# Performance work log

Hardware: AMD Instinct MI355X
Metric: run time of the kernel (lower is better)

Reference implementation:

```python
import math
import jax, jax.numpy as jnp
import numpy as np

D_MODEL = 1024
N_HEADS = 16
D_K = D_MODEL // N_HEADS


def _alibi_slopes(n_heads):
    # Faithful to the torch _get_slopes: slopes[i] = 2**(-8 + i), subsampled if
    # n_heads is not a power of two.
    power = 2 ** math.ceil(math.log2(n_heads))
    slopes = np.array([2.0 ** (-8 + i) for i in range(power)], dtype=np.float32)
    if n_heads != power:
        ratio = power // n_heads
        slopes = slopes[np.arange(0, power, ratio)][:n_heads]
    return jnp.asarray(slopes)


def setup_inputs() -> dict:
    key = jax.random.key(0)
    ks = jax.random.split(key, 11)
    B, S, D = 2, 2048, D_MODEL
    w = 0.02  # weight init scale
    return {
        "query": jax.random.normal(ks[0], (B, S, D), jnp.float32),
        "key": jax.random.normal(ks[1], (B, S, D), jnp.float32),
        "value": jax.random.normal(ks[2], (B, S, D), jnp.float32),
        "Wq": jax.random.normal(ks[3], (D, D), jnp.float32) * w,
        "bq": jax.random.normal(ks[4], (D,), jnp.float32) * w,
        "Wk": jax.random.normal(ks[5], (D, D), jnp.float32) * w,
        "bk": jax.random.normal(ks[6], (D,), jnp.float32) * w,
        "Wv": jax.random.normal(ks[7], (D, D), jnp.float32) * w,
        "bv": jax.random.normal(ks[8], (D,), jnp.float32) * w,
        "Wo": jax.random.normal(ks[9], (D, D), jnp.float32) * w,
        "bo": jax.random.normal(ks[10], (D,), jnp.float32) * w,
    }


def reference(query, key, value, Wq, bq, Wk, bk, Wv, bv, Wo, bo):
    B, Sq, D = query.shape
    Sk = key.shape[1]
    H, dk = N_HEADS, D_K

    # projections (torch Linear: x @ W.T + b)
    q = (query @ Wq.T + bq).reshape(B, Sq, H, dk).transpose(0, 2, 1, 3)  # [B,H,Sq,dk]
    k = (key @ Wk.T + bk).reshape(B, Sk, H, dk).transpose(0, 2, 1, 3)    # [B,H,Sk,dk]
    v = (value @ Wv.T + bv).reshape(B, Sk, H, dk).transpose(0, 2, 1, 3)  # [B,H,Sk,dk]

    scores = jnp.einsum("bhqd,bhkd->bhqk", q, k) / jnp.sqrt(jnp.float32(dk))

    # ALiBi bias: slopes[h] * (i - j), non-causal path (is_causal=False)
    dist = (jnp.arange(Sq)[:, None] - jnp.arange(Sk)[None, :]).astype(scores.dtype)
    slopes = _alibi_slopes(H)
    scores = scores + slopes[None, :, None, None] * dist[None, None, :, :]

    attn = jax.nn.softmax(scores, axis=-1)
    out = jnp.einsum("bhqk,bhkd->bhqd", attn, v)          # [B,H,Sq,dk]
    out = out.transpose(0, 2, 1, 3).reshape(B, Sq, D)     # [B,Sq,D]
    return out @ Wo.T + bo
```

## Files before the change

### kernel.cpp

```cpp
#include <hip/hip_runtime.h>

typedef __bf16 bf16_t;
typedef bf16_t bf16x8 __attribute__((ext_vector_type(8)));
typedef float f32x4 __attribute__((ext_vector_type(4)));
typedef float f32x16 __attribute__((ext_vector_type(16)));
typedef unsigned short u16x4 __attribute__((ext_vector_type(4)));
typedef unsigned int u32x4v __attribute__((ext_vector_type(4)));
typedef unsigned int u32;

#define DEV static __device__ __forceinline__


DEV unsigned short f2bf(float f) {
  unsigned int u = __builtin_bit_cast(unsigned int, f);
  u = (u + 0x7fffu + ((u >> 16) & 1u)) >> 16;
  return (unsigned short)u;
}

DEV float fexp2(float x) {
  float r;
  asm("v_exp_f32 %0, %1" : "=v"(r) : "v"(x));
  return r;
}

DEV u32 cvtpk(float lo, float hi_) {
  u32 r;
  asm("v_cvt_pk_bf16_f32 %0, %1, %2" : "=v"(r) : "v"(lo), "v"(hi_));
  return r;
}

DEV void plswap(u32& a, u32& b) {
  asm("v_permlane32_swap_b32 %0, %1" : "+v"(a), "+v"(b));
}

DEV void async_ld16(const unsigned short* gsrc, unsigned short* lbase, int lane) {
#if __has_builtin(__builtin_amdgcn_global_load_lds)
  __builtin_amdgcn_global_load_lds(
      (const __attribute__((address_space(1))) unsigned int*)(const void*)gsrc,
      (__attribute__((address_space(3))) unsigned int*)(void*)lbase, 16, 0, 0);
#else
  *reinterpret_cast<u32x4v*>(reinterpret_cast<char*>(lbase) + lane * 16) =
      *reinterpret_cast<const u32x4v*>(gsrc);
#endif
}


DEV void cvt_body(const float* __restrict__ src, unsigned short* __restrict__ dst, int i) {
  const float4* s = reinterpret_cast<const float4*>(src) + (size_t)i * 2;
  float4 a = s[0], c = s[1];
  u16x4 lo = {f2bf(a.x), f2bf(a.y), f2bf(a.z), f2bf(a.w)};
  u16x4 hi = {f2bf(c.x), f2bf(c.y), f2bf(c.z), f2bf(c.w)};
  u16x4* d = reinterpret_cast<u16x4*>(dst) + (size_t)i * 2;
  d[0] = lo;
  d[1] = hi;
}

__global__ __launch_bounds__(256) void cvt_qkv(const float* __restrict__ q,
                                               const float* __restrict__ k,
                                               const float* __restrict__ v,
                                               unsigned short* dq, unsigned short* dk,
                                               unsigned short* dv) {
  const int i = blockIdx.x * 256 + threadIdx.x;
  const float* src = blockIdx.z == 0 ? q : blockIdx.z == 1 ? k : v;
  unsigned short* dst = blockIdx.z == 0 ? dq : blockIdx.z == 1 ? dk : dv;
  cvt_body(src, dst, i);
}

__global__ __launch_bounds__(256) void cvt_w(const float* __restrict__ a,
                                             const float* __restrict__ b,
                                             const float* __restrict__ c,
                                             const float* __restrict__ d, unsigned short* da,
                                             unsigned short* db_, unsigned short* dc,
                                             unsigned short* dd) {
  const int i = blockIdx.x * 256 + threadIdx.x;
  const float* src = blockIdx.z == 0 ? a : blockIdx.z == 1 ? b : blockIdx.z == 2 ? c : d;
  unsigned short* dst = blockIdx.z == 0 ? da : blockIdx.z == 1 ? db_ : blockIdx.z == 2 ? dc : dd;
  cvt_body(src, dst, i);
}


DEV void stage_tile_128x64(const unsigned short* __restrict__ G, int row0, int k0,
                           unsigned short* lbuf, int lane, int wv) {
#pragma unroll
  for (int r = 0; r < 4; ++r) {
    const int rowA = (r * 4 + wv) * 8 + (lane >> 3);
    const int chunk = (lane & 7) ^ (rowA & 7);
    const unsigned short* gsrc = G + (size_t)(row0 + rowA) * 1024 + k0 + chunk * 8;
    unsigned short* lbase = lbuf + (r * 4 + wv) * 512;
    async_ld16(gsrc, lbase, lane);
  }
}

DEV void gemm_core(const unsigned short* __restrict__ X, const unsigned short* __restrict__ W,
                   unsigned short* lA, unsigned short* lB, int bm0, int bn0, int lane, int wv,
                   int wm, int wn, f32x4 acc[4][4]) {
  for (int kt = 0; kt < 16; ++kt) {
    __syncthreads();
    stage_tile_128x64(X, bm0, kt * 64, lA, lane, wv);
    stage_tile_128x64(W, bn0, kt * 64, lB, lane, wv);
    __syncthreads();
#pragma unroll
    for (int kk = 0; kk < 2; ++kk) {
      bf16x8 af[4], bfr[4];
#pragma unroll
      for (int f = 0; f < 4; ++f) {
        const int rowA = wm * 64 + f * 16 + (lane & 15);
        const int cA = (kk * 4 + (lane >> 4)) ^ (rowA & 7);
        af[f] = *reinterpret_cast<const bf16x8*>(lA + rowA * 64 + cA * 8);
        const int rowB = wn * 64 + f * 16 + (lane & 15);
        const int cB = (kk * 4 + (lane >> 4)) ^ (rowB & 7);
        bfr[f] = *reinterpret_cast<const bf16x8*>(lB + rowB * 64 + cB * 8);
      }
#pragma unroll
      for (int i = 0; i < 4; ++i)
#pragma unroll
        for (int j = 0; j < 4; ++j)
          acc[i][j] = __builtin_amdgcn_mfma_f32_16x16x32_bf16(af[i], bfr[j], acc[i][j], 0, 0, 0);
    }
  }
}


__global__ __launch_bounds__(256) void gemm_qkv_kernel(
    const unsigned short* __restrict__ Xq, const unsigned short* __restrict__ Xk,
    const unsigned short* __restrict__ Xv, const unsigned short* __restrict__ Wq,
    const unsigned short* __restrict__ Wk, const unsigned short* __restrict__ Wv,
    const float* __restrict__ bq, const float* __restrict__ bk, const float* __restrict__ bv,
    unsigned short* __restrict__ Qp, unsigned short* __restrict__ Kp,
    unsigned short* __restrict__ Vp) {
  __shared__ unsigned short lA[128 * 64];
  __shared__ unsigned short lB[128 * 64];
  const unsigned short* X;
  const unsigned short* W;
  const float* bias;
  unsigned short* dst;
  if (blockIdx.z == 0) { X = Xq; W = Wq; bias = bq; dst = Qp; }
  else if (blockIdx.z == 1) { X = Xk; W = Wk; bias = bk; dst = Kp; }
  else { X = Xv; W = Wv; bias = bv; dst = Vp; }
  const bool zV = (blockIdx.z == 2);
  const int lane = threadIdx.x & 63, wv = threadIdx.x >> 6;
  const int wm = wv >> 1, wn = wv & 1;
  const int bm0 = blockIdx.x * 128, bn0 = blockIdx.y * 128;
  f32x4 acc[4][4] = {};
  gemm_core(X, W, lA, lB, bm0, bn0, lane, wv, wm, wn, acc);
#pragma unroll
  for (int i = 0; i < 4; ++i) {
    const int mbase = bm0 + wm * 64 + i * 16 + ((lane >> 4) << 2);
#pragma unroll
    for (int j = 0; j < 4; ++j) {
      const int n = bn0 + wn * 64 + j * 16 + (lane & 15);
      const float bia = bias[n];
      const int h = n >> 6, d = n & 63;
#pragma unroll
      for (int r = 0; r < 4; ++r) {
        const int m = mbase + r;
        const int b = m >> 11, s = m & 2047;
        const unsigned short val = f2bf(acc[i][j][r] + bia);
        if (zV)
          dst[((size_t)(b * 16 + h) * 64 + d) * 2048 + s] = val;
        else
          dst[((size_t)(b * 16 + h) * 2048 + s) * 64 + d] = val;
      }
    }
  }
}


__global__ __launch_bounds__(256) void gemm_out_kernel(const unsigned short* __restrict__ X,
                                                       const unsigned short* __restrict__ W,
                                                       const float* __restrict__ bias,
                                                       float* __restrict__ out) {
  __shared__ unsigned short lA[128 * 64];
  __shared__ unsigned short lB[128 * 64];
  const int lane = threadIdx.x & 63, wv = threadIdx.x >> 6;
  const int wm = wv >> 1, wn = wv & 1;
  const int bm0 = blockIdx.x * 128, bn0 = blockIdx.y * 128;
  f32x4 acc[4][4] = {};
  gemm_core(X, W, lA, lB, bm0, bn0, lane, wv, wm, wn, acc);
#pragma unroll
  for (int i = 0; i < 4; ++i) {
    const int mbase = bm0 + wm * 64 + i * 16 + ((lane >> 4) << 2);
#pragma unroll
    for (int j = 0; j < 4; ++j) {
      const int n = bn0 + wn * 64 + j * 16 + (lane & 15);
      const float bia = bias[n];
#pragma unroll
      for (int r = 0; r < 4; ++r) out[(size_t)(mbase + r) * 1024 + n] = acc[i][j][r] + bia;
    }
  }
}


__global__ __launch_bounds__(256) void knorm_kernel(const unsigned short* __restrict__ Kp,
                                                    unsigned* __restrict__ nb2) {
  const int bh = blockIdx.y;
  const int s = blockIdx.x * 256 + threadIdx.x;
  const u32x4v* row = reinterpret_cast<const u32x4v*>(Kp + ((size_t)bh * 2048 + s) * 64);
  float ss = 0.0f;
#pragma unroll
  for (int c = 0; c < 8; ++c) {
    u32x4v u = row[c];
#pragma unroll
    for (int e = 0; e < 4; ++e) {
      const float lo = __builtin_bit_cast(float, u[e] << 16);
      const float hi = __builtin_bit_cast(float, u[e] & 0xFFFF0000u);
      ss = __builtin_fmaf(lo, lo, ss);
      ss = __builtin_fmaf(hi, hi, ss);
    }
  }
#pragma unroll
  for (int off = 1; off <= 32; off <<= 1) ss = fmaxf(ss, __shfl_xor(ss, off));
  if ((threadIdx.x & 63) == 0) atomicMax(nb2 + bh, __float_as_uint(ss));
}


__global__ __launch_bounds__(128) void attn_prepass(const unsigned short* __restrict__ Qp,
                                                    const unsigned short* __restrict__ Kp,
                                                    const unsigned* __restrict__ nb2,
                                                    float* __restrict__ mfA,
                                                    float* __restrict__ bltA) {
  __shared__ float sred[4];
  const int lane = threadIdx.x & 63, wv = threadIdx.x >> 6;
  const int lq = lane & 31, hi = lane >> 5;
  const int qt = blockIdx.x, bh = blockIdx.y, h = bh & 15;
  const float L2E = 1.4426950408889634f;
  const float slope2 = ldexpf(L2E, h - 8);
  const float SC2 = 0.125f * L2E;
  const size_t headoff = (size_t)bh * 2048 * 64;
  const unsigned short* Qh = Qp + headoff;
  const unsigned short* Kh = Kp + headoff;
  const int q_glob = qt * 64 + wv * 32 + lq;

  bf16x8 qf[4];
#pragma unroll
  for (int tt = 0; tt < 4; ++tt)
    qf[tt] = *reinterpret_cast<const bf16x8*>(Qh + (size_t)q_glob * 64 + tt * 16 + hi * 8);

  float qq = 0.0f;
#pragma unroll
  for (int tt = 0; tt < 4; ++tt)
#pragma unroll
    for (int e = 0; e < 8; ++e) {
      const float x = (float)qf[tt][e];
      qq = __builtin_fmaf(x, x, qq);
    }
  qq += __shfl_xor(qq, 32);
#pragma unroll
  for (int off = 1; off <= 16; off <<= 1) qq = fmaxf(qq, __shfl_xor(qq, off));

  f32x16 s0 = {}, s1 = {};
#pragma unroll
  for (int tt = 0; tt < 4; ++tt) {
    bf16x8 k0 = *reinterpret_cast<const bf16x8*>(Kh + (size_t)lq * 64 + tt * 16 + hi * 8);
    s0 = __builtin_amdgcn_mfma_f32_32x32x16_bf16(k0, qf[tt], s0, 0, 0, 0);
    bf16x8 k1 = *reinterpret_cast<const bf16x8*>(Kh + (size_t)(32 + lq) * 64 + tt * 16 + hi * 8);
    s1 = __builtin_amdgcn_mfma_f32_32x32x16_bf16(k1, qf[tt], s1, 0, 0, 0);
  }
  float zmax = -3.0e38f;
#pragma unroll
  for (int r = 0; r < 16; ++r) {
    const float cb = -slope2 * (float)(4 * hi + (r & 3) + 8 * (r >> 2));
    const float x0 = __builtin_fmaf(s0[r], SC2, cb);
    const float x1 = __builtin_fmaf(s1[r], SC2, cb - slope2 * 32.0f);
    zmax = fmaxf(zmax, fmaxf(x0, x1));
  }
  zmax = fmaxf(zmax, __shfl_xor(zmax, 32));
  float zmin = zmax;
#pragma unroll
  for (int off = 1; off <= 16; off <<= 1) zmin = fminf(zmin, __shfl_xor(zmin, off));
  if (lane == 0) {
    sred[wv] = zmin;
    sred[2 + wv] = qq;
  }
  __syncthreads();
  if (threadIdx.x == 0) {
    const float mf = fminf(sred[0], sred[1]);
    const float qn = sqrtf(fmaxf(sred[2], sred[3]));
    const float nk = sqrtf(__uint_as_float(nb2[bh]));
    mfA[bh * 32 + qt] = mf;
    bltA[bh * 32 + qt] = qn * nk * SC2;
  }
}


DEV void stage_tile64(const unsigned short* __restrict__ Gbase, size_t stride, int colbase,
                      unsigned short* lbuf, int lane, int wv) {
#pragma unroll
  for (int i = 0; i < 4; ++i) {
    const int r = i * 16 + wv * 8 + (lane >> 3);
    const int chunk = (lane & 7) ^ (r & 7);
    async_ld16(Gbase + (size_t)r * stride + colbase + chunk * 8, lbuf + (i * 16 + wv * 8) * 64,
               lane);
  }
}

__global__ __launch_bounds__(128) void attn_split_kernel(
    const unsigned short* __restrict__ Qp, const unsigned short* __restrict__ Kp,
    const unsigned short* __restrict__ VTp, const float* __restrict__ mfA,
    const float* __restrict__ bltA, float* __restrict__ ML, float* __restrict__ Opart, int Ct,
    int nsplit) {
  __shared__ unsigned short Kb[2][64 * 64];
  __shared__ unsigned short Vb[2][64 * 64];
  const int lane = threadIdx.x & 63, wv = threadIdx.x >> 6;
  const int lq = lane & 31, hi = lane >> 5;
  const int qt = blockIdx.x, sp = blockIdx.y, bh = blockIdx.z;
  const int h = bh & 15;
  const int idx = bh * 32 + qt;
  const float L2E = 1.4426950408889634f;
  const float slope2 = ldexpf(L2E, h - 8);
  const float SC2 = 0.125f * L2E;
  const float m_floor = mfA[idx], blt = bltA[idx];
  const float tf = (blt - m_floor + 34.0f) / (slope2 * 64.0f);
  const int T_act = min(32, (int)tf + 1);
  const int t0 = sp * Ct;
  const int nt = min(Ct, T_act - t0);
  float* mlb = ML + ((size_t)idx * nsplit + sp) * 128;
  if (nt <= 0) {
    mlb[threadIdx.x] = threadIdx.x < 64 ? -3.0e38f : 0.0f;
    return;
  }
  float* ob = Opart + ((size_t)idx * nsplit + sp) * 4096;
  const size_t headoff = (size_t)bh * 2048 * 64;
  const unsigned short* Qh = Qp + headoff;
  const unsigned short* Kh = Kp + headoff;
  const unsigned short* VTh = VTp + headoff;
  const int q_glob = qt * 64 + wv * 32 + lq;

  float cb0[16], cb1[16];
#pragma unroll
  for (int r = 0; r < 16; ++r) {
    cb0[r] = -slope2 * (float)(4 * hi + (r & 3) + 8 * (r >> 2));
    cb1[r] = cb0[r] - slope2 * 32.0f;
  }

  bf16x8 qf[4];
#pragma unroll
  for (int tt = 0; tt < 4; ++tt)
    qf[tt] = *reinterpret_cast<const bf16x8*>(Qh + (size_t)q_glob * 64 + tt * 16 + hi * 8);

  stage_tile64(Kh + (size_t)(t0 * 64) * 64, 64, 0, Kb[0], lane, wv);
  stage_tile64(VTh, 2048, t0 * 64, Vb[0], lane, wv);
  __syncthreads();

  f32x16 acc0 = {}, acc1 = {};
  float m_run = m_floor, l_run = 0.0f;

  for (int ti = 0; ti < nt; ++ti) {
    const int kv0 = (t0 + ti) * 64;
    const float s2k = slope2 * (float)kv0;
    const unsigned short* Kc = Kb[ti & 1];
    const unsigned short* Vc = Vb[ti & 1];
    if (ti + 1 < nt) {
      stage_tile64(Kh + (size_t)(kv0 + 64) * 64, 64, 0, Kb[(ti + 1) & 1], lane, wv);
      stage_tile64(VTh, 2048, kv0 + 64, Vb[(ti + 1) & 1], lane, wv);
    }
    f32x16 s0 = {}, s1 = {};
    __builtin_amdgcn_s_setprio(1);
#pragma unroll
    for (int tt = 0; tt < 4; ++tt) {
      {
        const int row = lq;
        const int ch = (tt * 2 + hi) ^ (row & 7);
        bf16x8 kf = *reinterpret_cast<const bf16x8*>(Kc + row * 64 + ch * 8);
        s0 = __builtin_amdgcn_mfma_f32_32x32x16_bf16(kf, qf[tt], s0, 0, 0, 0);
      }
      {
        const int row = 32 + lq;
        const int ch = (tt * 2 + hi) ^ (row & 7);
        bf16x8 kf = *reinterpret_cast<const bf16x8*>(Kc + row * 64 + ch * 8);
        s1 = __builtin_amdgcn_mfma_f32_32x32x16_bf16(kf, qf[tt], s1, 0, 0, 0);
      }
    }
    __builtin_amdgcn_s_setprio(0);
    float zmax = -3.0e38f;
#pragma unroll
    for (int r = 0; r < 16; ++r) {
      s0[r] = __builtin_fmaf(s0[r], SC2, cb0[r]);
      s1[r] = __builtin_fmaf(s1[r], SC2, cb1[r]);
      zmax = fmaxf(zmax, fmaxf(s0[r], s1[r]));
    }
    zmax = fmaxf(zmax, __shfl_xor(zmax, 32));
    const float tmax_true = zmax - s2k;
    if (__any(tmax_true > m_run + 8.0f)) {
      const float m_new = fmaxf(m_run, tmax_true);
      const float alpha = fexp2(m_run - m_new);
      m_run = m_new;
      l_run *= alpha;
      acc0 *= alpha;
      acc1 *= alpha;
    }
    const float mm = m_run + s2k;
    float ps0 = 0.0f, ps1 = 0.0f;
#pragma unroll
    for (int r = 0; r < 16; ++r) {
      const float p0 = fexp2(s0[r] - mm);
      const float p1 = fexp2(s1[r] - mm);
      s0[r] = p0;
      s1[r] = p1;
      ps0 += p0;
      ps1 += p1;
    }
    float psum = ps0 + ps1;
    psum += __shfl_xor(psum, 32);
    l_run += psum;
    bf16x8 pf[4];
#pragma unroll
    for (int half = 0; half < 2; ++half) {
      u32 w0 = cvtpk(s0[half * 8 + 0], s0[half * 8 + 1]);
      u32 w2 = cvtpk(s0[half * 8 + 4], s0[half * 8 + 5]);
      plswap(w0, w2);
      u32 w1 = cvtpk(s0[half * 8 + 2], s0[half * 8 + 3]);
      u32 w3 = cvtpk(s0[half * 8 + 6], s0[half * 8 + 7]);
      plswap(w1, w3);
      u32x4v ww = {w0, w1, w2, w3};
      pf[half] = __builtin_bit_cast(bf16x8, ww);
    }
#pragma unroll
    for (int half = 0; half < 2; ++half) {
      u32 w0 = cvtpk(s1[half * 8 + 0], s1[half * 8 + 1]);
      u32 w2 = cvtpk(s1[half * 8 + 4], s1[half * 8 + 5]);
      plswap(w0, w2);
      u32 w1 = cvtpk(s1[half * 8 + 2], s1[half * 8 + 3]);
      u32 w3 = cvtpk(s1[half * 8 + 6], s1[half * 8 + 7]);
      plswap(w1, w3);
      u32x4v ww = {w0, w1, w2, w3};
      pf[2 + half] = __builtin_bit_cast(bf16x8, ww);
    }
    __builtin_amdgcn_s_setprio(1);
#pragma unroll
    for (int tt = 0; tt < 4; ++tt) {
      {
        const int row = lq;
        const int ch = (tt * 2 + hi) ^ (row & 7);
        bf16x8 vf = *reinterpret_cast<const bf16x8*>(Vc + row * 64 + ch * 8);
        acc0 = __builtin_amdgcn_mfma_f32_32x32x16_bf16(vf, pf[tt], acc0, 0, 0, 0);
      }
      {
        const int row = 32 + lq;
        const int ch = (tt * 2 + hi) ^ (row & 7);
        bf16x8 vf = *reinterpret_cast<const bf16x8*>(Vc + row * 64 + ch * 8);
        acc1 = __builtin_amdgcn_mfma_f32_32x32x16_bf16(vf, pf[tt], acc1, 0, 0, 0);
      }
    }
    __builtin_amdgcn_s_setprio(0);
    __syncthreads();
  }
  const int qloc = wv * 32 + lq;
  if (hi == 0) {
    mlb[qloc] = m_run;
    mlb[64 + qloc] = l_run;
  }
#pragma unroll
  for (int g = 0; g < 4; ++g) {
    f32x4 w0, w1;
#pragma unroll
    for (int e = 0; e < 4; ++e) {
      w0[e] = acc0[g * 4 + e];
      w1[e] = acc1[g * 4 + e];
    }
    *reinterpret_cast<f32x4*>(ob + qloc * 64 + g * 8 + 4 * hi) = w0;
    *reinterpret_cast<f32x4*>(ob + qloc * 64 + 32 + g * 8 + 4 * hi) = w1;
  }
}


__global__ __launch_bounds__(256) void attn_combine(const float* __restrict__ ML,
                                                    const float* __restrict__ Opart,
                                                    unsigned short* __restrict__ Ob, int nsplit) {
  const int idx = blockIdx.x;
  const int bh = idx >> 5, qt = idx & 31;
  const int h = bh & 15, b = bh >> 4;
  const int q = threadIdx.x >> 2, d0 = (threadIdx.x & 3) * 16;
  const float* mlb = ML + (size_t)idx * nsplit * 128;
  const float* ob = Opart + (size_t)idx * nsplit * 4096;
  float m_g = -3.0e38f;
  for (int s = 0; s < nsplit; ++s) m_g = fmaxf(m_g, mlb[s * 128 + q]);
  float l = 0.0f;
  f32x4 acc[4] = {};
  for (int s = 0; s < nsplit; ++s) {
    const float ms = mlb[s * 128 + q], ls = mlb[s * 128 + 64 + q];
    const float w = fexp2(ms - m_g);
    const float wl = w * ls;
    if (wl > 0.0f) {
      l += wl;
      const f32x4* src = reinterpret_cast<const f32x4*>(ob + (size_t)s * 4096 + q * 64 + d0);
#pragma unroll
      for (int j = 0; j < 4; ++j) {
        f32x4 v = src[j];
#pragma unroll
        for (int e = 0; e < 4; ++e) acc[j][e] = __builtin_fmaf(w, v[e], acc[j][e]);
      }
    }
  }
  const float invl = 1.0f / l;
  unsigned short* orow = Ob + ((size_t)(b * 2048 + qt * 64 + q)) * 1024 + h * 64 + d0;
#pragma unroll
  for (int j = 0; j < 4; ++j) {
    u16x4 pk;
#pragma unroll
    for (int e = 0; e < 4; ++e) pk[e] = f2bf(acc[j][e] * invl);
    *reinterpret_cast<u16x4*>(orow + j * 4) = pk;
  }
}


extern "C" void kernel_launch(void* const* d_in, const int* in_sizes, int n_in, void* d_out,
                              int out_size, void* d_ws, size_t ws_size, hipStream_t stream) {
  const float* q = (const float*)d_in[0];
  const float* k = (const float*)d_in[1];
  const float* v = (const float*)d_in[2];
  const float* Wq = (const float*)d_in[3];
  const float* bq = (const float*)d_in[4];
  const float* Wk = (const float*)d_in[5];
  const float* bk = (const float*)d_in[6];
  const float* Wv = (const float*)d_in[7];
  const float* bv = (const float*)d_in[8];
  const float* Wo = (const float*)d_in[9];
  const float* bo = (const float*)d_in[10];

  char* ws = (char*)d_ws;
  const size_t MB = 1024 * 1024;
  unsigned short* qb = (unsigned short*)(ws + 0 * MB);
  unsigned short* kb = (unsigned short*)(ws + 8 * MB);
  unsigned short* vb = (unsigned short*)(ws + 16 * MB);
  unsigned short* Wqb = (unsigned short*)(ws + 24 * MB);
  unsigned short* Wkb = (unsigned short*)(ws + 26 * MB);
  unsigned short* Wvb = (unsigned short*)(ws + 28 * MB);
  unsigned short* Wob = (unsigned short*)(ws + 30 * MB);
  unsigned short* Qp = (unsigned short*)(ws + 32 * MB);
  unsigned short* Kp = (unsigned short*)(ws + 40 * MB);
  unsigned short* VTp = (unsigned short*)(ws + 48 * MB);
  unsigned short* Obf = (unsigned short*)(ws + 0 * MB);

  int nsplit;
  float *nb2f, *mfA, *bltA, *ML, *Opart;
  if (ws_size >= (size_t)121 * MB) nsplit = 4;
  else if (ws_size >= (size_t)89 * MB) nsplit = 2;
  else nsplit = 1;
  if (ws_size >= (size_t)73 * MB) {
    nb2f = (float*)(ws + 24 * MB);
    mfA = (float*)(ws + 24 * MB + 4096);
    bltA = (float*)(ws + 24 * MB + 8192);
    ML = (float*)(ws + 26 * MB);
    Opart = (float*)(ws + 56 * MB);
  } else {
    nsplit = 1;
    nb2f = (float*)(ws + 26 * MB);
    mfA = (float*)(ws + 26 * MB + 4096);
    bltA = (float*)(ws + 26 * MB + 8192);
    ML = (float*)(ws + 26 * MB + 65536);
    Opart = (float*)(ws + 8 * MB);
  }
  const int Ct = 32 / nsplit;

  cvt_qkv<<<dim3(2048, 1, 3), 256, 0, stream>>>(q, k, v, qb, kb, vb);
  cvt_w<<<dim3(512, 1, 4), 256, 0, stream>>>(Wq, Wk, Wv, Wo, Wqb, Wkb, Wvb, Wob);

  gemm_qkv_kernel<<<dim3(32, 8, 3), 256, 0, stream>>>(qb, kb, vb, Wqb, Wkb, Wvb, bq, bk, bv, Qp,
                                                      Kp, VTp);
  hipMemsetAsync(nb2f, 0, 32 * sizeof(float), stream);
  knorm_kernel<<<dim3(8, 32), 256, 0, stream>>>(Kp, (unsigned*)nb2f);
  attn_prepass<<<dim3(32, 32), 128, 0, stream>>>(Qp, Kp, (const unsigned*)nb2f, mfA, bltA);
  attn_split_kernel<<<dim3(32, nsplit, 32), 128, 0, stream>>>(Qp, Kp, VTp, mfA, bltA, ML, Opart,
                                                              Ct, nsplit);
  attn_combine<<<1024, 256, 0, stream>>>(ML, Opart, Obf, nsplit);
  gemm_out_kernel<<<dim3(32, 8), 256, 0, stream>>>(Obf, Wob, bo, (float*)d_out);
}
```

Before: 141.2 us.

## Triple-buffer GEMM LDS tiles with async prefetch and XCD-aware block swizzle

The projection GEMMs now use 128x32 K-slices held in a three-stage LDS ring. Loads for step k+2 are issued while step k computes, and a single barrier plus a partial vmcnt wait replaces the two syncthreads per tile. Block indices are remapped so that consecutive blocks land on the same chiplet for better L2 reuse, and launch bounds request 3 blocks per CU. This is meant to hide global-load latency, at the cost of fragile hand-written waitcnt logic and a changed swizzle pattern.

```diff
diff --git a/kernel.cpp b/kernel.cpp
--- a/kernel.cpp
+++ b/kernel.cpp
@@ -79,70 +79,96 @@
 }
 
 
-DEV void stage_tile_128x64(const unsigned short* __restrict__ G, int row0, int k0,
+DEV void stage_tile_128x32(const unsigned short* __restrict__ G, int row0, int k0,
                            unsigned short* lbuf, int lane, int wv) {
-#pragma unroll
-  for (int r = 0; r < 4; ++r) {
-    const int rowA = (r * 4 + wv) * 8 + (lane >> 3);
-    const int chunk = (lane & 7) ^ (rowA & 7);
-    const unsigned short* gsrc = G + (size_t)(row0 + rowA) * 1024 + k0 + chunk * 8;
-    unsigned short* lbase = lbuf + (r * 4 + wv) * 512;
-    async_ld16(gsrc, lbase, lane);
-  }
+  const int gch = (lane & 3) ^ ((lane >> 3) & 3);
+  const int rr = wv * 16 + (lane >> 2);
+#pragma unroll
+  for (int r = 0; r < 2; ++r)
+    async_ld16(G + (size_t)(row0 + r * 64 + rr) * 1024 + k0 + gch * 8,
+               lbuf + (r * 64 + wv * 16) * 32, lane);
+}
+
+DEV void gstep(const unsigned short* __restrict__ X, const unsigned short* __restrict__ W,
+               int bm0, int bn0, int k2, const unsigned short* cA, const unsigned short* cB,
+               unsigned short* nA, unsigned short* nB, int lane, int wv, int offa, int offb,
+               int lastmode, f32x4 acc[4][4]) {
+  if (lastmode == 0)
+    asm volatile("s_waitcnt vmcnt(4)" ::: "memory");
+  else
+    asm volatile("s_waitcnt vmcnt(0)" ::: "memory");
+  __builtin_amdgcn_s_barrier();
+  if (k2 < 1024) {
+    stage_tile_128x32(X, bm0, k2, nA, lane, wv);
+    stage_tile_128x32(W, bn0, k2, nB, lane, wv);
+  }
+  bf16x8 af[4], bfr[4];
+#pragma unroll
+  for (int f = 0; f < 4; ++f) {
+    af[f] = *reinterpret_cast<const bf16x8*>(cA + offa + f * 512);
+    bfr[f] = *reinterpret_cast<const bf16x8*>(cB + offb + f * 512);
+  }
+#pragma unroll
+  for (int i = 0; i < 4; ++i)
+#pragma unroll
+    for (int j = 0; j < 4; ++j)
+      acc[i][j] = __builtin_amdgcn_mfma_f32_16x16x32_bf16(af[i], bfr[j], acc[i][j], 0, 0, 0);
 }
 
 DEV void gemm_core(const unsigned short* __restrict__ X, const unsigned short* __restrict__ W,
-                   unsigned short* lA, unsigned short* lB, int bm0, int bn0, int lane, int wv,
-                   int wm, int wn, f32x4 acc[4][4]) {
-  for (int kt = 0; kt < 16; ++kt) {
-    __syncthreads();
-    stage_tile_128x64(X, bm0, kt * 64, lA, lane, wv);
-    stage_tile_128x64(W, bn0, kt * 64, lB, lane, wv);
-    __syncthreads();
-#pragma unroll
-    for (int kk = 0; kk < 2; ++kk) {
-      bf16x8 af[4], bfr[4];
-#pragma unroll
-      for (int f = 0; f < 4; ++f) {
-        const int rowA = wm * 64 + f * 16 + (lane & 15);
-        const int cA = (kk * 4 + (lane >> 4)) ^ (rowA & 7);
-        af[f] = *reinterpret_cast<const bf16x8*>(lA + rowA * 64 + cA * 8);
-        const int rowB = wn * 64 + f * 16 + (lane & 15);
-        const int cB = (kk * 4 + (lane >> 4)) ^ (rowB & 7);
-        bfr[f] = *reinterpret_cast<const bf16x8*>(lB + rowB * 64 + cB * 8);
-      }
-#pragma unroll
-      for (int i = 0; i < 4; ++i)
-#pragma unroll
-        for (int j = 0; j < 4; ++j)
-          acc[i][j] = __builtin_amdgcn_mfma_f32_16x16x32_bf16(af[i], bfr[j], acc[i][j], 0, 0, 0);
-    }
-  }
-}
-
-
-__global__ __launch_bounds__(256) void gemm_qkv_kernel(
+                   unsigned short* lds, int bm0, int bn0, int lane, int wv, int wm, int wn,
+                   f32x4 acc[4][4]) {
+  unsigned short* A0 = lds;
+  unsigned short* A1 = lds + 4096;
+  unsigned short* A2 = lds + 8192;
+  unsigned short* B0 = lds + 12288;
+  unsigned short* B1 = lds + 16384;
+  unsigned short* B2 = lds + 20480;
+  const int ch = (lane >> 4) ^ (((lane & 15) >> 1) & 3);
+  const int offa = (wm * 64 + (lane & 15)) * 32 + ch * 8;
+  const int offb = (wn * 64 + (lane & 15)) * 32 + ch * 8;
+  stage_tile_128x32(X, bm0, 0, A0, lane, wv);
+  stage_tile_128x32(W, bn0, 0, B0, lane, wv);
+  stage_tile_128x32(X, bm0, 32, A1, lane, wv);
+  stage_tile_128x32(W, bn0, 32, B1, lane, wv);
+#pragma unroll 1
+  for (int kt = 0; kt < 30; kt += 3) {
+    gstep(X, W, bm0, bn0, (kt + 2) * 32, A0, B0, A2, B2, lane, wv, offa, offb, 0, acc);
+    gstep(X, W, bm0, bn0, (kt + 3) * 32, A1, B1, A0, B0, lane, wv, offa, offb, 0, acc);
+    gstep(X, W, bm0, bn0, (kt + 4) * 32, A2, B2, A1, B1, lane, wv, offa, offb, 0, acc);
+  }
+  gstep(X, W, bm0, bn0, 1024, A0, B0, A2, B2, lane, wv, offa, offb, 0, acc);
+  gstep(X, W, bm0, bn0, 1056, A1, B1, A2, B2, lane, wv, offa, offb, 1, acc);
+}
+
+
+__global__ __launch_bounds__(256, 3) void gemm_qkv_kernel(
     const unsigned short* __restrict__ Xq, const unsigned short* __restrict__ Xk,
     const unsigned short* __restrict__ Xv, const unsigned short* __restrict__ Wq,
     const unsigned short* __restrict__ Wk, const unsigned short* __restrict__ Wv,
     const float* __restrict__ bq, const float* __restrict__ bk, const float* __restrict__ bv,
     unsigned short* __restrict__ Qp, unsigned short* __restrict__ Kp,
     unsigned short* __restrict__ Vp) {
-  __shared__ unsigned short lA[128 * 64];
-  __shared__ unsigned short lB[128 * 64];
+  __shared__ unsigned short lds[24576];
+  const int flat = blockIdx.x + 32 * blockIdx.y + 256 * blockIdx.z;
+  const int swz = (flat & 7) * 96 + (flat >> 3);
+  const int bx = swz & 31;
+  const int rest = swz >> 5;
+  const int by = rest & 7;
+  const int bz = rest >> 3;
   const unsigned short* X;
   const unsigned short* W;
   const float* bias;
   unsigned short* dst;
-  if (blockIdx.z == 0) { X = Xq; W = Wq; bias = bq; dst = Qp; }
-  else if (blockIdx.z == 1) { X = Xk; W = Wk; bias = bk; dst = Kp; }
+  if (bz == 0) { X = Xq; W = Wq; bias = bq; dst = Qp; }
+  else if (bz == 1) { X = Xk; W = Wk; bias = bk; dst = Kp; }
   else { X = Xv; W = Wv; bias = bv; dst = Vp; }
-  const bool zV = (blockIdx.z == 2);
+  const bool zV = (bz == 2);
   const int lane = threadIdx.x & 63, wv = threadIdx.x >> 6;
   const int wm = wv >> 1, wn = wv & 1;
-  const int bm0 = blockIdx.x * 128, bn0 = blockIdx.y * 128;
+  const int bm0 = bx * 128, bn0 = by * 128;
   f32x4 acc[4][4] = {};
-  gemm_core(X, W, lA, lB, bm0, bn0, lane, wv, wm, wn, acc);
+  gemm_core(X, W, lds, bm0, bn0, lane, wv, wm, wn, acc);
 #pragma unroll
   for (int i = 0; i < 4; ++i) {
     const int mbase = bm0 + wm * 64 + i * 16 + ((lane >> 4) << 2);
@@ -166,17 +192,19 @@
 }
 
 
-__global__ __launch_bounds__(256) void gemm_out_kernel(const unsigned short* __restrict__ X,
-                                                       const unsigned short* __restrict__ W,
-                                                       const float* __restrict__ bias,
-                                                       float* __restrict__ out) {
-  __shared__ unsigned short lA[128 * 64];
-  __shared__ unsigned short lB[128 * 64];
+__global__ __launch_bounds__(256, 3) void gemm_out_kernel(const unsigned short* __restrict__ X,
+                                                          const unsigned short* __restrict__ W,
+                                                          const float* __restrict__ bias,
+                                                          float* __restrict__ out) {
+  __shared__ unsigned short lds[24576];
+  const int flat = blockIdx.x + 32 * blockIdx.y;
+  const int swz = (flat & 7) * 32 + (flat >> 3);
+  const int bx = swz & 31, by = swz >> 5;
   const int lane = threadIdx.x & 63, wv = threadIdx.x >> 6;
   const int wm = wv >> 1, wn = wv & 1;
-  const int bm0 = blockIdx.x * 128, bn0 = blockIdx.y * 128;
+  const int bm0 = bx * 128, bn0 = by * 128;
   f32x4 acc[4][4] = {};
-  gemm_core(X, W, lA, lB, bm0, bn0, lane, wv, wm, wn, acc);
+  gemm_core(X, W, lds, bm0, bn0, lane, wv, wm, wn, acc);
 #pragma unroll
   for (int i = 0; i < 4; ++i) {
     const int mbase = bm0 + wm * 64 + i * 16 + ((lane >> 4) << 2);
```

After: 140.8 us. About the same (-0.3%).
